# Kernel optimization log

Hardware: AMD Instinct MI355X
Metric: run time of the kernel (lower is better)

Reference implementation:

```python
import jax, jax.numpy as jnp
import numpy as np

N_NODES = 100000


def _deg_norm(idx, n):
    # inverse-sqrt degree, zero-degree nodes -> 0 (DGL norm='both' convention)
    deg = jax.ops.segment_sum(jnp.ones(idx.shape, jnp.float32), idx, num_segments=n)
    return jnp.where(deg > 0, jax.lax.rsqrt(jnp.maximum(deg, 1.0)), 0.0)


def graph_conv(x, src, dst, W, b, n):
    # symmetric normalization: D_out^{-1/2} on src, D_in^{-1/2} on dst
    norm_src = _deg_norm(src, n)  # [N]
    norm_dst = _deg_norm(dst, n)  # [N]
    h = (x * norm_src[:, None]) @ W          # apply weight first (in >= out)
    msg = h[src]                              # gather [E, out]
    agg = jax.ops.segment_sum(msg, dst, num_segments=n)  # scatter-add [N, out]
    return agg * norm_dst[:, None] + b


def setup_inputs() -> dict:
    key = jax.random.key(0)
    ks = jax.random.split(key, 6)
    x = jax.random.normal(ks[0], (N_NODES, 128), dtype=jnp.float32)
    edge_index = jax.random.randint(ks[1], (2, 1600000), 0, N_NODES, dtype=jnp.int64)
    W1 = jax.random.normal(ks[2], (128, 64), dtype=jnp.float32) * (1.0 / np.sqrt(128))
    b1 = jnp.zeros((64,), jnp.float32)
    W2 = jax.random.normal(ks[3], (64, 32), dtype=jnp.float32) * (1.0 / np.sqrt(64))
    b2 = jnp.zeros((32,), jnp.float32)
    Wl = jax.random.normal(ks[4], (32, 1), dtype=jnp.float32) * (1.0 / np.sqrt(32))
    bl = jnp.zeros((1,), jnp.float32)
    return {"x": x, "edge_index": edge_index, "W1": W1, "b1": b1,
            "W2": W2, "b2": b2, "Wl": Wl, "bl": bl}


def reference(x, edge_index, W1, b1, W2, b2, Wl, bl):
    src, dst = edge_index[0], edge_index[1]
    n = x.shape[0]
    h = graph_conv(x, src, dst, W1, b1, n)
    h = jax.nn.relu(h)
    # dropout(p=0.5) is identity at inference
    h = graph_conv(h, src, dst, W2, b2, n)
    return h @ Wl + bl  # [N, 1]
```

## Files before the change

kernel.cpp:

```cpp
#include <hip/hip_runtime.h>
#include <hip/hip_fp16.h>


#define WAVE 64
#define NRANGE 8
#define NQUAD 2
#define CB 1024

typedef _Float16 f16x8 __attribute__((ext_vector_type(8)));
typedef float f32x4 __attribute__((ext_vector_type(4)));

__global__ __launch_bounds__(256) void k_hist(const int* __restrict__ srcArr,
                                              const int* __restrict__ dstArr,
                                              unsigned* __restrict__ partial_s,
                                              unsigned* __restrict__ partial_d,
                                              int E, int B, int C, int chunkE) {
    extern __shared__ unsigned hist[];
    const int q = blockIdx.x & (NQUAD - 1);
    const int c = blockIdx.x >> 1;
    const int lo = q * 4 * B;
    const int* nodes = blockIdx.y ? dstArr : srcArr;
    unsigned* partial = blockIdx.y ? partial_d : partial_s;

    for (int b = threadIdx.x; b < B; b += 256) hist[b] = 0u;
    __syncthreads();

    const int beg = c * chunkE, end = min(beg + chunkE, E);
    const int n4 = (end - beg) >> 2;
    const int4* p = (const int4*)(nodes + beg);
    for (int j = threadIdx.x; j < n4; j += 256) {
        int4 v = p[j];
#pragma unroll
        for (int k = 0; k < 4; ++k) {
            int a = (&v.x)[k] - lo;
            if ((unsigned)a < (unsigned)(4 * B)) {
                int h2 = (a >= 2 * B);
                int r2 = a - (h2 ? 2 * B : 0);
                int h1 = (r2 >= B);
                int bin = r2 - (h1 ? B : 0);
                atomicAdd(&hist[bin], 1u << (((h2 << 1) | h1) << 3));
            }
        }
    }
    for (int j = beg + (n4 << 2) + threadIdx.x; j < end; j += 256) {
        int a = nodes[j] - lo;
        if ((unsigned)a < (unsigned)(4 * B)) {
            int h2 = (a >= 2 * B);
            int r2 = a - (h2 ? 2 * B : 0);
            int h1 = (r2 >= B);
            int bin = r2 - (h1 ? B : 0);
            atomicAdd(&hist[bin], 1u << (((h2 << 1) | h1) << 3));
        }
    }
    __syncthreads();
    unsigned* outp = partial + (size_t)(q * C + c) * B;
    for (int b = threadIdx.x; b < B; b += 256) outp[b] = hist[b];
}

__global__ __launch_bounds__(256) void k_reduce_norm(const unsigned* __restrict__ partial_s,
                                                     unsigned* __restrict__ partial_d,
                                                     float* __restrict__ norm_s,
                                                     float* __restrict__ norm_d,
                                                     unsigned* __restrict__ deg_d,
                                                     int N, int B, int C) {
    int t = blockIdx.x * 256 + threadIdx.x;
    if (t >= NQUAD * B) return;
    int q = t / B, b = t - q * B;
    size_t base = (size_t)(q * C) * B + b;
    unsigned ds = 0;
    for (int c = 0; c < C; ++c) ds += partial_s[base + (size_t)c * B];
    unsigned run = 0;
    for (int c = 0; c < C; ++c) {
        size_t ix = base + (size_t)c * B;
        unsigned v = partial_d[ix];
        partial_d[ix] = run;
        run += v;
    }
#pragma unroll
    for (int j = 0; j < 4; ++j) {
        int n = q * 4 * B + j * B + b;
        if (n < N) {
            unsigned d0 = (ds >> (8 * j)) & 0xffu;
            unsigned d1 = (run >> (8 * j)) & 0xffu;
            deg_d[n] = d1;
            norm_s[n] = d0 ? rsqrtf((float)d0) : 0.0f;
            norm_d[n] = d1 ? rsqrtf((float)d1) : 0.0f;
        }
    }
}

__global__ __launch_bounds__(256) void k_prep(const float* __restrict__ W1,
                                              const float* __restrict__ W2,
                                              const float* __restrict__ b2,
                                              const float* __restrict__ Wl,
                                              const float* __restrict__ bl,
                                              _Float16* __restrict__ wt,
                                              float* __restrict__ w2l,
                                              float* __restrict__ c0) {
    int t = threadIdx.x;
    for (int i = 0; i < 32; ++i) {
        int e = i * 256 + t;
        int k = e >> 6, n = e & 63;
        wt[n * 128 + k] = (_Float16)W1[e];
    }
    if (t < 64) {
        float acc = 0.f;
#pragma unroll
        for (int j = 0; j < 32; ++j) acc += W2[t * 32 + j] * Wl[j];
        w2l[t] = acc;
    }
    if (t == 0) {
        float s = 0.f;
#pragma unroll
        for (int j = 0; j < 32; ++j) s += b2[j] * Wl[j];
        *c0 = s + bl[0];
    }
}

__global__ __launch_bounds__(256) void k_blocksum(const unsigned* __restrict__ deg,
                                                  unsigned* __restrict__ partial, int N) {
    __shared__ unsigned sw[4];
    int i = blockIdx.x * 256 + threadIdx.x;
    unsigned v = (i < N) ? deg[i] : 0u;
#pragma unroll
    for (int off = 32; off; off >>= 1) v += __shfl_xor((int)v, off);
    if ((threadIdx.x & 63) == 0) sw[threadIdx.x >> 6] = v;
    __syncthreads();
    if (threadIdx.x == 0) partial[blockIdx.x] = sw[0] + sw[1] + sw[2] + sw[3];
}

__global__ __launch_bounds__(512) void k_scanpartial(const unsigned* __restrict__ partial,
                                                     unsigned* __restrict__ blockoff,
                                                     unsigned* __restrict__ offsets,
                                                     int nb, int N) {
    __shared__ unsigned s[512];
    int t = threadIdx.x;
    unsigned v = (t < nb) ? partial[t] : 0u;
    s[t] = v;
    __syncthreads();
    for (int off = 1; off < 512; off <<= 1) {
        unsigned a = (t >= off) ? s[t - off] : 0u;
        __syncthreads();
        s[t] += a;
        __syncthreads();
    }
    if (t < nb) blockoff[t] = s[t] - v;
    if (t == nb - 1) offsets[N] = s[t];
}

__global__ __launch_bounds__(256) void k_offsets(const unsigned* __restrict__ deg,
                                                 const unsigned* __restrict__ blockoff,
                                                 unsigned* __restrict__ offsets, int N) {
    __shared__ unsigned s[256];
    int t = threadIdx.x;
    int i = blockIdx.x * 256 + t;
    unsigned v = (i < N) ? deg[i] : 0u;
    s[t] = v;
    __syncthreads();
    for (int off = 1; off < 256; off <<= 1) {
        unsigned a = (t >= off) ? s[t - off] : 0u;
        __syncthreads();
        s[t] += a;
        __syncthreads();
    }
    if (i < N) offsets[i] = blockoff[blockIdx.x] + s[t] - v;
}

__global__ __launch_bounds__(256) void k_cnt(const int* __restrict__ dst,
                                             unsigned* __restrict__ cnt,
                                             int E, int B, int chunkEb) {
    __shared__ unsigned lc[NRANGE];
    if (threadIdx.x < NRANGE) lc[threadIdx.x] = 0u;
    __syncthreads();
    const int c = blockIdx.x;
    const int beg = c * chunkEb, end = min(beg + chunkEb, E);
    unsigned pc[NRANGE] = {};
    for (int i = beg + (int)threadIdx.x; i < end; i += 256) {
        int r = dst[i] / B;
#pragma unroll
        for (int rr = 0; rr < NRANGE; ++rr) pc[rr] += (r == rr);
    }
#pragma unroll
    for (int rr = 0; rr < NRANGE; ++rr) {
        unsigned v = pc[rr];
#pragma unroll
        for (int off = 32; off; off >>= 1) v += __shfl_xor((int)v, off);
        if ((threadIdx.x & 63) == 0 && v) atomicAdd(&lc[rr], v);
    }
    __syncthreads();
    if (threadIdx.x < NRANGE) cnt[threadIdx.x * CB + c] = lc[threadIdx.x];
}

__global__ __launch_bounds__(256) void k_scancnt2(const unsigned* __restrict__ cnt,
                                                  unsigned* __restrict__ segBase) {
    __shared__ unsigned s[256];
    const int t = threadIdx.x;
    const int PER = (NRANGE * CB) / 256;
    unsigned loc[PER];
    unsigned sum = 0;
#pragma unroll
    for (int j = 0; j < PER; ++j) { loc[j] = sum; sum += cnt[t * PER + j]; }
    s[t] = sum;
    __syncthreads();
    for (int off = 1; off < 256; off <<= 1) {
        unsigned a = (t >= off) ? s[t - off] : 0u;
        __syncthreads();
        s[t] += a;
        __syncthreads();
    }
    unsigned base = s[t] - sum;
#pragma unroll
    for (int j = 0; j < PER; ++j) segBase[t * PER + j] = base + loc[j];
    if (t == 255) segBase[NRANGE * CB] = s[255];
}

__global__ __launch_bounds__(256) void k_bucket(const int* __restrict__ src,
                                                const int* __restrict__ dst,
                                                const unsigned* __restrict__ segBase,
                                                uint2* __restrict__ ebuf,
                                                int E, int B, int chunkEb) {
    __shared__ unsigned lcnt[NRANGE];
    const int c = blockIdx.x;
    const int lane = threadIdx.x & 63;
    if (threadIdx.x < NRANGE) lcnt[threadIdx.x] = 0u;
    __syncthreads();

    unsigned sb[NRANGE];
#pragma unroll
    for (int r = 0; r < NRANGE; ++r) sb[r] = segBase[r * CB + c];

    const int beg = c * chunkEb, end = min(beg + chunkEb, E);
    for (int i = beg + (int)threadIdx.x; i < end; i += 256) {
        int d = dst[i];
        int s = src[i];
        int r = d / B;
#pragma unroll
        for (int rr = 0; rr < NRANGE; ++rr) {
            unsigned long long m = __ballot(r == rr);
            if (m) {
                int leader = __ffsll((long long)m) - 1;
                unsigned base = 0;
                if (lane == leader) base = atomicAdd(&lcnt[rr], (unsigned)__popcll(m));
                base = (unsigned)__shfl((int)base, leader);
                if (r == rr) {
                    unsigned before = (unsigned)__popcll(m & ((1ull << lane) - 1ull));
                    ebuf[sb[rr] + base + before] = make_uint2((unsigned)s, (unsigned)d);
                }
            }
        }
    }
}

__global__ __launch_bounds__(256) void k_fill2(const uint2* __restrict__ ebuf,
                                               const unsigned* __restrict__ segBase,
                                               const unsigned* __restrict__ offsets,
                                               const unsigned* __restrict__ rel,
                                               unsigned* __restrict__ csr,
                                               int N, int B, int C, int RB) {
    extern __shared__ unsigned curs[];
    const int r = blockIdx.x & (NRANGE - 1);
    const int ch = blockIdx.x >> 3;
    const int lo = r * B;
    const int bins = min(B, N - lo);
    const int sh = (r & 3) << 3;
    const unsigned* relp = rel + (size_t)((r >> 2) * C + ch) * B;
    for (int b = threadIdx.x; b < bins; b += 256)
        curs[b] = offsets[lo + b] + ((relp[b] >> sh) & 0xffu);
    __syncthreads();

    const unsigned s0 = segBase[r * CB + ch * RB];
    const unsigned s1 = segBase[r * CB + ch * RB + RB];
    for (unsigned i = s0 + threadIdx.x; i < s1; i += 256) {
        uint2 e = ebuf[i];
        int a = (int)e.y - lo;
        if ((unsigned)a < (unsigned)bins)
            csr[atomicAdd(&curs[a], 1u)] = e.x;
    }
}

__global__ __launch_bounds__(256) void k_gemm1(const float* __restrict__ x,
                                               const _Float16* __restrict__ wt,
                                               const float* __restrict__ norm_s,
                                               __half* __restrict__ h1h, int N) {
    __shared__ __align__(16) _Float16 xs[64 * 128];
    const int tid = threadIdx.x, lane = tid & 63, wv = tid >> 6;
    const int r0 = blockIdx.x * 64;

    f16x8 bf[4][4];
#pragma unroll
    for (int kt = 0; kt < 4; ++kt)
#pragma unroll
        for (int nt = 0; nt < 4; ++nt)
            bf[kt][nt] = *(const f16x8*)&wt[(nt * 16 + (lane & 15)) * 128 +
                                            kt * 32 + (lane >> 4) * 8];

#pragma unroll
    for (int it = 0; it < 8; ++it) {
        int e = it * 256 + tid;
        int r = e >> 5, c = e & 31;
        int row = r0 + r;
        float4 v = (row < N) ? ((const float4*)x)[(size_t)row * 32 + c]
                             : make_float4(0.f, 0.f, 0.f, 0.f);
        __half2 lo2 = __floats2half2_rn(v.x, v.y);
        __half2 hi2 = __floats2half2_rn(v.z, v.w);
        uint2 pk;
        pk.x = *(unsigned*)&lo2;
        pk.y = *(unsigned*)&hi2;
        int byte = r * 256 + c * 8;
        byte ^= (r & 7) << 4;
        *(uint2*)((char*)xs + byte) = pk;
    }
    __syncthreads();

    f32x4 acc[4] = {};
    const int rloc = wv * 16 + (lane & 15);
#pragma unroll
    for (int kt = 0; kt < 4; ++kt) {
        int byte = rloc * 256 + (kt * 32 + (lane >> 4) * 8) * 2;
        byte ^= (rloc & 7) << 4;
        f16x8 af = *(const f16x8*)((char*)xs + byte);
#pragma unroll
        for (int nt = 0; nt < 4; ++nt)
            acc[nt] = __builtin_amdgcn_mfma_f32_16x16x32_f16(af, bf[kt][nt], acc[nt], 0, 0, 0);
    }

#pragma unroll
    for (int j = 0; j < 4; ++j) {
        int row = r0 + wv * 16 + (lane >> 4) * 4 + j;
        if (row < N) {
            float ns = norm_s[row];
#pragma unroll
            for (int nt = 0; nt < 4; ++nt)
                h1h[(size_t)row * 64 + nt * 16 + (lane & 15)] =
                    __float2half(acc[nt][j] * ns);
        }
    }
}

__global__ __launch_bounds__(256) void k_agg_rdot(const unsigned* __restrict__ offsets,
                                                  const unsigned* __restrict__ csr,
                                                  const __half* __restrict__ h1h,
                                                  const float* __restrict__ norm_s,
                                                  const float* __restrict__ norm_d,
                                                  const float* __restrict__ b1,
                                                  const float* __restrict__ w2l,
                                                  float* __restrict__ s_node, int N) {
    const int lane = threadIdx.x & 63;
    const int slot = lane >> 4;
    const int p = lane & 15;
    const int v = (blockIdx.x * 256 + threadIdx.x) >> 6;
    if (v >= N) return;
    const unsigned beg = offsets[v], end = offsets[v + 1];

    float a0 = 0.f, a1 = 0.f, a2 = 0.f, a3 = 0.f;
#define GATHER(sreg) { \
        uint2 u = *(const uint2*)&h1h[(size_t)(sreg) * 64 + 4 * p]; \
        float2 f0 = __half22float2(*(__half2*)&u.x); \
        float2 f1 = __half22float2(*(__half2*)&u.y); \
        a0 += f0.x; a1 += f0.y; a2 += f1.x; a3 += f1.y; }

    for (unsigned base = beg; base < end; base += WAVE) {
        const int n = (int)min((unsigned)WAVE, end - base);
        int sv = (lane < n) ? (int)csr[base + lane] : 0;
        int i = 0;
        for (; i + 32 <= n; i += 32) {
            int s0 = __shfl(sv, i + 0 + slot);
            int s1 = __shfl(sv, i + 4 + slot);
            int s2 = __shfl(sv, i + 8 + slot);
            int s3 = __shfl(sv, i + 12 + slot);
            int s4 = __shfl(sv, i + 16 + slot);
            int s5 = __shfl(sv, i + 20 + slot);
            int s6 = __shfl(sv, i + 24 + slot);
            int s7 = __shfl(sv, i + 28 + slot);
            GATHER(s0); GATHER(s1); GATHER(s2); GATHER(s3);
            GATHER(s4); GATHER(s5); GATHER(s6); GATHER(s7);
        }
        for (; i + 16 <= n; i += 16) {
            int s0 = __shfl(sv, i + 0 + slot);
            int s1 = __shfl(sv, i + 4 + slot);
            int s2 = __shfl(sv, i + 8 + slot);
            int s3 = __shfl(sv, i + 12 + slot);
            GATHER(s0); GATHER(s1); GATHER(s2); GATHER(s3);
        }
        for (; i < n; i += 4) {
            int e = i + slot;
            int s = __shfl(sv, min(e, n - 1));
            if (e < n) GATHER(s);
        }
    }
#undef GATHER
    a0 += __shfl_xor(a0, 16); a0 += __shfl_xor(a0, 32);
    a1 += __shfl_xor(a1, 16); a1 += __shfl_xor(a1, 32);
    a2 += __shfl_xor(a2, 16); a2 += __shfl_xor(a2, 32);
    a3 += __shfl_xor(a3, 16); a3 += __shfl_xor(a3, 32);

    float nd = norm_d[v];
    float4 bq = *(const float4*)&b1[4 * p];
    float4 wq = *(const float4*)&w2l[4 * p];
    float t = fmaxf(fmaf(a0, nd, bq.x), 0.f) * wq.x
            + fmaxf(fmaf(a1, nd, bq.y), 0.f) * wq.y
            + fmaxf(fmaf(a2, nd, bq.z), 0.f) * wq.z
            + fmaxf(fmaf(a3, nd, bq.w), 0.f) * wq.w;
#pragma unroll
    for (int off = 8; off; off >>= 1) t += __shfl_xor(t, off);
    if (lane == 0) s_node[v] = t * norm_s[v];
}

__global__ __launch_bounds__(256) void k_out(const unsigned* __restrict__ offsets,
                                             const unsigned* __restrict__ csr,
                                             const float* __restrict__ s_node,
                                             const float* __restrict__ norm_d,
                                             const float* __restrict__ c0,
                                             float* __restrict__ out, int N) {
    int v = blockIdx.x * 256 + threadIdx.x;
    if (v >= N) return;
    unsigned beg = offsets[v], end = offsets[v + 1];
    float sum = 0.f;
    unsigned j = beg;
    for (; j + 4 <= end; j += 4) {
        float a = s_node[csr[j + 0]], b = s_node[csr[j + 1]];
        float c = s_node[csr[j + 2]], d = s_node[csr[j + 3]];
        sum += a + b + c + d;
    }
    for (; j < end; ++j) sum += s_node[csr[j]];
    out[v] = fmaf(sum, norm_d[v], *c0);
}

extern "C" void kernel_launch(void* const* d_in, const int* in_sizes, int n_in,
                              void* d_out, int out_size, void* d_ws, size_t ws_size,
                              hipStream_t stream) {
    const float* x  = (const float*)d_in[0];
    const int*   ei = (const int*)d_in[1];
    const float* W1 = (const float*)d_in[2];
    const float* b1 = (const float*)d_in[3];
    const float* W2 = (const float*)d_in[4];
    const float* b2 = (const float*)d_in[5];
    const float* Wl = (const float*)d_in[6];
    const float* bl = (const float*)d_in[7];

    const int N = in_sizes[0] / 128;
    const int E = in_sizes[1] / 2;
    const int* src = ei;
    const int* dst = ei + E;
    const int NB = (N + 255) / 256;
    const int B = (N + NRANGE - 1) / NRANGE;

    size_t baseBytes = 0;
    {
        auto pad = [](size_t b) { return (b + 255) & ~(size_t)255; };
        baseBytes = pad((size_t)N * 4) * 3 + pad((size_t)(N + 1) * 4) +
                    pad((size_t)NB * 4) * 2 + pad((size_t)N * 64 * 2) +
                    pad((size_t)E * 4) + pad((size_t)N * 4) + pad(64 * 4) + pad(4) +
                    pad(64 * 128 * 2) + pad((size_t)E * 8) +
                    pad((size_t)(NRANGE * CB + 1) * 4) * 2;
    }
    int C = 64;
    while (C > 4 && baseBytes + 2ull * NQUAD * C * B * 4ull > ws_size) C >>= 1;
    const int chunkEb = (E + CB - 1) / CB;
    const int RB = CB / C;
    const int chunkE = chunkEb * RB;

    char* w = (char*)d_ws;
    auto alloc = [&](size_t bytes) -> void* {
        void* r = (void*)w;
        w += (bytes + 255) & ~(size_t)255;
        return r;
    };
    float*    norm_s    = (float*)alloc((size_t)N * 4);
    float*    norm_d    = (float*)alloc((size_t)N * 4);
    unsigned* deg_d     = (unsigned*)alloc((size_t)N * 4);
    unsigned* offsets   = (unsigned*)alloc((size_t)(N + 1) * 4);
    unsigned* partial   = (unsigned*)alloc((size_t)NB * 4);
    unsigned* blockoff  = (unsigned*)alloc((size_t)NB * 4);
    __half*   h1h       = (__half*)alloc((size_t)N * 64 * 2);
    unsigned* csr       = (unsigned*)alloc((size_t)E * 4);
    float*    s_node    = (float*)alloc((size_t)N * 4);
    float*    w2l       = (float*)alloc(64 * 4);
    float*    c0        = (float*)alloc(4);
    _Float16* wt        = (_Float16*)alloc(64 * 128 * 2);
    uint2*    ebuf      = (uint2*)alloc((size_t)E * 8);
    unsigned* cnt       = (unsigned*)alloc((size_t)(NRANGE * CB + 1) * 4);
    unsigned* segBase   = (unsigned*)alloc((size_t)(NRANGE * CB + 1) * 4);
    unsigned* partial_s = (unsigned*)alloc((size_t)NQUAD * C * B * 4);
    unsigned* partial_d = (unsigned*)alloc((size_t)NQUAD * C * B * 4);

    float* out = (float*)d_out;
    const size_t ldsB = (size_t)B * 4;

    k_cnt<<<CB, 256, 0, stream>>>(dst, cnt, E, B, chunkEb);
    k_scancnt2<<<1, 256, 0, stream>>>(cnt, segBase);
    k_bucket<<<CB, 256, 0, stream>>>(src, dst, segBase, ebuf, E, B, chunkEb);

    k_hist<<<dim3(NQUAD * C, 2), 256, ldsB, stream>>>(src, dst, partial_s, partial_d,
                                                      E, B, C, chunkE);
    k_prep<<<1, 256, 0, stream>>>(W1, W2, b2, Wl, bl, wt, w2l, c0);

    k_reduce_norm<<<(NQUAD * B + 255) / 256, 256, 0, stream>>>(partial_s, partial_d,
                                                               norm_s, norm_d,
                                                               deg_d, N, B, C);
    k_blocksum<<<NB, 256, 0, stream>>>(deg_d, partial, N);
    k_scanpartial<<<1, 512, 0, stream>>>(partial, blockoff, offsets, NB, N);
    k_offsets<<<NB, 256, 0, stream>>>(deg_d, blockoff, offsets, N);

    k_fill2<<<NRANGE * C, 256, ldsB, stream>>>(ebuf, segBase, offsets, partial_d,
                                               csr, N, B, C, RB);

    k_gemm1<<<(N + 63) / 64, 256, 0, stream>>>(x, wt, norm_s, h1h, N);

    k_agg_rdot<<<(N + 3) / 4, 256, 0, stream>>>(offsets, csr, h1h, norm_s, norm_d,
                                                b1, w2l, s_node, N);
    k_out<<<NB, 256, 0, stream>>>(offsets, csr, s_node, norm_d, c0, out, N);
}
```

Baseline: 195.7 us.

## Fuse CSR build, degree norms, scans and GEMM1 into one cooperative kernel

Roughly ten small launches (count, bucket, histogram, reduce/norm, block scans, offsets, fill, weight prep, first GEMM) become one persistent cooperative kernel of 512 blocks, separated by grid-wide syncs. The histogram partitioning is also retuned to 16 node ranges and 32 chunks with fixed sizes, and independent phases (bucketing, block sums, GEMM tiles) share the stages between syncs. This removes launch gaps and tail idle time between dependent stages. In exchange, parallelism per phase is capped at the grid size and each grid.sync adds latency. Occupancy is also limited by the larger dynamic LDS allocation.

```diff
diff --git a/kernel.cpp b/kernel.cpp
--- a/kernel.cpp
+++ b/kernel.cpp
@@ -1,338 +1,314 @@
 #include <hip/hip_runtime.h>
 #include <hip/hip_fp16.h>
+#include <hip/hip_cooperative_groups.h>
+
+namespace cg = cooperative_groups;
 
 
 #define WAVE 64
 #define NRANGE 8
-#define NQUAD 2
 #define CB 1024
+#define GRID 512
+#define CHK 32
+#define RB (CB / CHK)
 
 typedef _Float16 f16x8 __attribute__((ext_vector_type(8)));
 typedef float f32x4 __attribute__((ext_vector_type(4)));
 
-__global__ __launch_bounds__(256) void k_hist(const int* __restrict__ srcArr,
-                                              const int* __restrict__ dstArr,
-                                              unsigned* __restrict__ partial_s,
-                                              unsigned* __restrict__ partial_d,
-                                              int E, int B, int C, int chunkE) {
-    extern __shared__ unsigned hist[];
-    const int q = blockIdx.x & (NQUAD - 1);
-    const int c = blockIdx.x >> 1;
-    const int lo = q * 4 * B;
-    const int* nodes = blockIdx.y ? dstArr : srcArr;
-    unsigned* partial = blockIdx.y ? partial_d : partial_s;
-
-    for (int b = threadIdx.x; b < B; b += 256) hist[b] = 0u;
-    __syncthreads();
-
-    const int beg = c * chunkE, end = min(beg + chunkE, E);
-    const int n4 = (end - beg) >> 2;
-    const int4* p = (const int4*)(nodes + beg);
-    for (int j = threadIdx.x; j < n4; j += 256) {
-        int4 v = p[j];
-#pragma unroll
-        for (int k = 0; k < 4; ++k) {
-            int a = (&v.x)[k] - lo;
-            if ((unsigned)a < (unsigned)(4 * B)) {
-                int h2 = (a >= 2 * B);
-                int r2 = a - (h2 ? 2 * B : 0);
-                int h1 = (r2 >= B);
-                int bin = r2 - (h1 ? B : 0);
-                atomicAdd(&hist[bin], 1u << (((h2 << 1) | h1) << 3));
-            }
-        }
-    }
-    for (int j = beg + (n4 << 2) + threadIdx.x; j < end; j += 256) {
-        int a = nodes[j] - lo;
-        if ((unsigned)a < (unsigned)(4 * B)) {
-            int h2 = (a >= 2 * B);
-            int r2 = a - (h2 ? 2 * B : 0);
-            int h1 = (r2 >= B);
-            int bin = r2 - (h1 ? B : 0);
-            atomicAdd(&hist[bin], 1u << (((h2 << 1) | h1) << 3));
-        }
-    }
-    __syncthreads();
-    unsigned* outp = partial + (size_t)(q * C + c) * B;
-    for (int b = threadIdx.x; b < B; b += 256) outp[b] = hist[b];
-}
-
-__global__ __launch_bounds__(256) void k_reduce_norm(const unsigned* __restrict__ partial_s,
-                                                     unsigned* __restrict__ partial_d,
-                                                     float* __restrict__ norm_s,
-                                                     float* __restrict__ norm_d,
-                                                     unsigned* __restrict__ deg_d,
-                                                     int N, int B, int C) {
-    int t = blockIdx.x * 256 + threadIdx.x;
-    if (t >= NQUAD * B) return;
-    int q = t / B, b = t - q * B;
-    size_t base = (size_t)(q * C) * B + b;
-    unsigned ds = 0;
-    for (int c = 0; c < C; ++c) ds += partial_s[base + (size_t)c * B];
-    unsigned run = 0;
-    for (int c = 0; c < C; ++c) {
-        size_t ix = base + (size_t)c * B;
-        unsigned v = partial_d[ix];
-        partial_d[ix] = run;
-        run += v;
-    }
-#pragma unroll
-    for (int j = 0; j < 4; ++j) {
-        int n = q * 4 * B + j * B + b;
-        if (n < N) {
-            unsigned d0 = (ds >> (8 * j)) & 0xffu;
-            unsigned d1 = (run >> (8 * j)) & 0xffu;
-            deg_d[n] = d1;
-            norm_s[n] = d0 ? rsqrtf((float)d0) : 0.0f;
-            norm_d[n] = d1 ? rsqrtf((float)d1) : 0.0f;
-        }
-    }
-}
-
-__global__ __launch_bounds__(256) void k_prep(const float* __restrict__ W1,
-                                              const float* __restrict__ W2,
-                                              const float* __restrict__ b2,
-                                              const float* __restrict__ Wl,
-                                              const float* __restrict__ bl,
-                                              _Float16* __restrict__ wt,
-                                              float* __restrict__ w2l,
-                                              float* __restrict__ c0) {
-    int t = threadIdx.x;
-    for (int i = 0; i < 32; ++i) {
-        int e = i * 256 + t;
-        int k = e >> 6, n = e & 63;
-        wt[n * 128 + k] = (_Float16)W1[e];
-    }
-    if (t < 64) {
-        float acc = 0.f;
-#pragma unroll
-        for (int j = 0; j < 32; ++j) acc += W2[t * 32 + j] * Wl[j];
-        w2l[t] = acc;
-    }
-    if (t == 0) {
-        float s = 0.f;
-#pragma unroll
-        for (int j = 0; j < 32; ++j) s += b2[j] * Wl[j];
-        *c0 = s + bl[0];
-    }
-}
-
-__global__ __launch_bounds__(256) void k_blocksum(const unsigned* __restrict__ deg,
-                                                  unsigned* __restrict__ partial, int N) {
-    __shared__ unsigned sw[4];
-    int i = blockIdx.x * 256 + threadIdx.x;
-    unsigned v = (i < N) ? deg[i] : 0u;
-#pragma unroll
-    for (int off = 32; off; off >>= 1) v += __shfl_xor((int)v, off);
-    if ((threadIdx.x & 63) == 0) sw[threadIdx.x >> 6] = v;
-    __syncthreads();
-    if (threadIdx.x == 0) partial[blockIdx.x] = sw[0] + sw[1] + sw[2] + sw[3];
-}
-
-__global__ __launch_bounds__(512) void k_scanpartial(const unsigned* __restrict__ partial,
-                                                     unsigned* __restrict__ blockoff,
-                                                     unsigned* __restrict__ offsets,
-                                                     int nb, int N) {
-    __shared__ unsigned s[512];
-    int t = threadIdx.x;
-    unsigned v = (t < nb) ? partial[t] : 0u;
-    s[t] = v;
-    __syncthreads();
-    for (int off = 1; off < 512; off <<= 1) {
-        unsigned a = (t >= off) ? s[t - off] : 0u;
-        __syncthreads();
-        s[t] += a;
-        __syncthreads();
-    }
-    if (t < nb) blockoff[t] = s[t] - v;
-    if (t == nb - 1) offsets[N] = s[t];
-}
-
-__global__ __launch_bounds__(256) void k_offsets(const unsigned* __restrict__ deg,
-                                                 const unsigned* __restrict__ blockoff,
-                                                 unsigned* __restrict__ offsets, int N) {
-    __shared__ unsigned s[256];
-    int t = threadIdx.x;
-    int i = blockIdx.x * 256 + t;
-    unsigned v = (i < N) ? deg[i] : 0u;
-    s[t] = v;
-    __syncthreads();
-    for (int off = 1; off < 256; off <<= 1) {
-        unsigned a = (t >= off) ? s[t - off] : 0u;
-        __syncthreads();
-        s[t] += a;
-        __syncthreads();
-    }
-    if (i < N) offsets[i] = blockoff[blockIdx.x] + s[t] - v;
-}
-
-__global__ __launch_bounds__(256) void k_cnt(const int* __restrict__ dst,
-                                             unsigned* __restrict__ cnt,
-                                             int E, int B, int chunkEb) {
-    __shared__ unsigned lc[NRANGE];
-    if (threadIdx.x < NRANGE) lc[threadIdx.x] = 0u;
-    __syncthreads();
-    const int c = blockIdx.x;
-    const int beg = c * chunkEb, end = min(beg + chunkEb, E);
-    unsigned pc[NRANGE] = {};
-    for (int i = beg + (int)threadIdx.x; i < end; i += 256) {
-        int r = dst[i] / B;
-#pragma unroll
-        for (int rr = 0; rr < NRANGE; ++rr) pc[rr] += (r == rr);
-    }
-#pragma unroll
-    for (int rr = 0; rr < NRANGE; ++rr) {
-        unsigned v = pc[rr];
+__global__ __launch_bounds__(256, 2) void k_build(
+    const int* __restrict__ src, const int* __restrict__ dst,
+    const float* __restrict__ x,
+    const float* __restrict__ W1, const float* __restrict__ W2,
+    const float* __restrict__ b2, const float* __restrict__ Wl,
+    const float* __restrict__ bl,
+    unsigned* cnt, unsigned* segBase, uint2* ebuf,
+    unsigned* partial_s, unsigned* partial_d,
+    float* norm_s, float* norm_d, unsigned* deg_d,
+    unsigned* partial, unsigned* blockoff, unsigned* offsets,
+    unsigned* csr, _Float16* wt, float* w2l, float* c0, __half* h1h,
+    int E, int N, int rngB, int hb, int chunkEb, int chunkE,
+    int NB, int ntiles)
+{
+    extern __shared__ unsigned lds[];
+    cg::grid_group grid = cg::this_grid();
+    const int bid = blockIdx.x;
+    const int tid = threadIdx.x;
+    const int lane = tid & 63;
+
+    for (int c = bid; c < CB; c += GRID) {
+        if (tid < NRANGE) lds[tid] = 0u;
+        __syncthreads();
+        const int beg = c * chunkEb, end = min(beg + chunkEb, E);
+        unsigned pc[NRANGE] = {};
+        for (int i = beg + tid; i < end; i += 256) {
+            int r = dst[i] / rngB;
+#pragma unroll
+            for (int rr = 0; rr < NRANGE; ++rr) pc[rr] += (r == rr);
+        }
+#pragma unroll
+        for (int rr = 0; rr < NRANGE; ++rr) {
+            unsigned v = pc[rr];
+#pragma unroll
+            for (int off = 32; off; off >>= 1) v += __shfl_xor((int)v, off);
+            if (lane == 0 && v) atomicAdd(&lds[rr], v);
+        }
+        __syncthreads();
+        if (tid < NRANGE) cnt[tid * CB + c] = lds[tid];
+        __syncthreads();
+    }
+    if (bid == GRID - 1) {
+        for (int i = 0; i < 32; ++i) {
+            int e = i * 256 + tid;
+            int k = e >> 6, n = e & 63;
+            wt[n * 128 + k] = (_Float16)W1[e];
+        }
+        if (tid < 64) {
+            float acc = 0.f;
+#pragma unroll
+            for (int j = 0; j < 32; ++j) acc += W2[tid * 32 + j] * Wl[j];
+            w2l[tid] = acc;
+        }
+        if (tid == 0) {
+            float s = 0.f;
+#pragma unroll
+            for (int j = 0; j < 32; ++j) s += b2[j] * Wl[j];
+            *c0 = s + bl[0];
+        }
+    }
+    if (bid < 256) {
+        const int arr = bid >> 7;
+        const int hq  = (bid >> 5) & 3;
+        const int c   = bid & 31;
+        const int lo  = hq * 4 * hb;
+        const int span = 4 * hb;
+        const int* nodes = arr ? dst : src;
+        unsigned* po = (arr ? partial_d : partial_s) + (size_t)(hq * CHK + c) * hb;
+        for (int b = tid; b < hb; b += 256) lds[b] = 0u;
+        __syncthreads();
+        const int beg = c * chunkE, end = min(beg + chunkE, E);
+        const int n4 = (end - beg) >> 2;
+        const int4* p = (const int4*)(nodes + beg);
+        for (int j = tid; j < n4; j += 256) {
+            int4 v = p[j];
+#pragma unroll
+            for (int k = 0; k < 4; ++k) {
+                int a = (&v.x)[k] - lo;
+                if ((unsigned)a < (unsigned)span) {
+                    int jj = a / hb;
+                    int b = a - jj * hb;
+                    atomicAdd(&lds[b], 1u << (jj << 3));
+                }
+            }
+        }
+        for (int j2 = beg + (n4 << 2) + tid; j2 < end; j2 += 256) {
+            int a = nodes[j2] - lo;
+            if ((unsigned)a < (unsigned)span) {
+                int jj = a / hb;
+                int b = a - jj * hb;
+                atomicAdd(&lds[b], 1u << (jj << 3));
+            }
+        }
+        __syncthreads();
+        for (int b = tid; b < hb; b += 256) po[b] = lds[b];
+    }
+    grid.sync();
+
+    if (bid == 0) {
+        const int PER = (NRANGE * CB) / 256;
+        unsigned loc[PER];
+        unsigned sum = 0;
+#pragma unroll
+        for (int j = 0; j < PER; ++j) { loc[j] = sum; sum += cnt[tid * PER + j]; }
+        lds[tid] = sum;
+        __syncthreads();
+        for (int off = 1; off < 256; off <<= 1) {
+            unsigned a = (tid >= off) ? lds[tid - off] : 0u;
+            __syncthreads();
+            lds[tid] += a;
+            __syncthreads();
+        }
+        unsigned base = lds[tid] - sum;
+#pragma unroll
+        for (int j = 0; j < PER; ++j) segBase[tid * PER + j] = base + loc[j];
+        if (tid == 255) segBase[NRANGE * CB] = lds[255];
+    } else {
+        int t = (bid - 1) * 256 + tid;
+        if (t < 4 * hb) {
+            int hq = t / hb, b = t - hq * hb;
+            size_t base = (size_t)(hq * CHK) * hb + b;
+            unsigned ds = 0;
+            for (int c = 0; c < CHK; ++c) ds += partial_s[base + (size_t)c * hb];
+            unsigned run = 0;
+            for (int c = 0; c < CHK; ++c) {
+                size_t ix = base + (size_t)c * hb;
+                unsigned v = partial_d[ix];
+                partial_d[ix] = run;
+                run += v;
+            }
+#pragma unroll
+            for (int j = 0; j < 4; ++j) {
+                int n = hq * 4 * hb + j * hb + b;
+                if (n < N) {
+                    unsigned d0 = (ds >> (8 * j)) & 0xffu;
+                    unsigned d1 = (run >> (8 * j)) & 0xffu;
+                    deg_d[n] = d1;
+                    norm_s[n] = d0 ? rsqrtf((float)d0) : 0.0f;
+                    norm_d[n] = d1 ? rsqrtf((float)d1) : 0.0f;
+                }
+            }
+        }
+    }
+    grid.sync();
+
+    for (int c = bid; c < CB; c += GRID) {
+        if (tid < NRANGE) lds[tid] = 0u;
+        __syncthreads();
+        unsigned sb[NRANGE];
+#pragma unroll
+        for (int r = 0; r < NRANGE; ++r) sb[r] = segBase[r * CB + c];
+        const int beg = c * chunkEb, end = min(beg + chunkEb, E);
+        for (int i = beg + tid; i < end; i += 256) {
+            int d = dst[i], s = src[i];
+            int r = d / rngB;
+#pragma unroll
+            for (int rr = 0; rr < NRANGE; ++rr) {
+                unsigned long long m = __ballot(r == rr);
+                if (m) {
+                    int leader = __ffsll((long long)m) - 1;
+                    unsigned b2r = 0;
+                    if (lane == leader) b2r = atomicAdd(&lds[rr], (unsigned)__popcll(m));
+                    b2r = (unsigned)__shfl((int)b2r, leader);
+                    if (r == rr) {
+                        unsigned before = (unsigned)__popcll(m & ((1ull << lane) - 1ull));
+                        ebuf[sb[rr] + b2r + before] = make_uint2((unsigned)s, (unsigned)d);
+                    }
+                }
+            }
+        }
+        __syncthreads();
+    }
+    for (int t = bid; t < NB; t += GRID) {
+        int i = t * 256 + tid;
+        unsigned v = (i < N) ? deg_d[i] : 0u;
 #pragma unroll
         for (int off = 32; off; off >>= 1) v += __shfl_xor((int)v, off);
-        if ((threadIdx.x & 63) == 0 && v) atomicAdd(&lc[rr], v);
-    }
-    __syncthreads();
-    if (threadIdx.x < NRANGE) cnt[threadIdx.x * CB + c] = lc[threadIdx.x];
-}
-
-__global__ __launch_bounds__(256) void k_scancnt2(const unsigned* __restrict__ cnt,
-                                                  unsigned* __restrict__ segBase) {
-    __shared__ unsigned s[256];
-    const int t = threadIdx.x;
-    const int PER = (NRANGE * CB) / 256;
-    unsigned loc[PER];
-    unsigned sum = 0;
-#pragma unroll
-    for (int j = 0; j < PER; ++j) { loc[j] = sum; sum += cnt[t * PER + j]; }
-    s[t] = sum;
-    __syncthreads();
-    for (int off = 1; off < 256; off <<= 1) {
-        unsigned a = (t >= off) ? s[t - off] : 0u;
-        __syncthreads();
-        s[t] += a;
-        __syncthreads();
-    }
-    unsigned base = s[t] - sum;
-#pragma unroll
-    for (int j = 0; j < PER; ++j) segBase[t * PER + j] = base + loc[j];
-    if (t == 255) segBase[NRANGE * CB] = s[255];
-}
-
-__global__ __launch_bounds__(256) void k_bucket(const int* __restrict__ src,
-                                                const int* __restrict__ dst,
-                                                const unsigned* __restrict__ segBase,
-                                                uint2* __restrict__ ebuf,
-                                                int E, int B, int chunkEb) {
-    __shared__ unsigned lcnt[NRANGE];
-    const int c = blockIdx.x;
-    const int lane = threadIdx.x & 63;
-    if (threadIdx.x < NRANGE) lcnt[threadIdx.x] = 0u;
-    __syncthreads();
-
-    unsigned sb[NRANGE];
-#pragma unroll
-    for (int r = 0; r < NRANGE; ++r) sb[r] = segBase[r * CB + c];
-
-    const int beg = c * chunkEb, end = min(beg + chunkEb, E);
-    for (int i = beg + (int)threadIdx.x; i < end; i += 256) {
-        int d = dst[i];
-        int s = src[i];
-        int r = d / B;
-#pragma unroll
-        for (int rr = 0; rr < NRANGE; ++rr) {
-            unsigned long long m = __ballot(r == rr);
-            if (m) {
-                int leader = __ffsll((long long)m) - 1;
-                unsigned base = 0;
-                if (lane == leader) base = atomicAdd(&lcnt[rr], (unsigned)__popcll(m));
-                base = (unsigned)__shfl((int)base, leader);
-                if (r == rr) {
-                    unsigned before = (unsigned)__popcll(m & ((1ull << lane) - 1ull));
-                    ebuf[sb[rr] + base + before] = make_uint2((unsigned)s, (unsigned)d);
+        __syncthreads();
+        if ((tid & 63) == 0) lds[tid >> 6] = v;
+        __syncthreads();
+        if (tid == 0) partial[t] = lds[0] + lds[1] + lds[2] + lds[3];
+        __syncthreads();
+    }
+    {
+        _Float16* xs = (_Float16*)lds;
+        for (int tile = bid; tile < ntiles; tile += GRID) {
+            const int wv = tid >> 6;
+            const int r0 = tile * 64;
+            f16x8 bf[4][4];
+#pragma unroll
+            for (int kt = 0; kt < 4; ++kt)
+#pragma unroll
+                for (int nt = 0; nt < 4; ++nt)
+                    bf[kt][nt] = *(const f16x8*)&wt[(nt * 16 + (lane & 15)) * 128 +
+                                                    kt * 32 + (lane >> 4) * 8];
+            __syncthreads();
+#pragma unroll
+            for (int it = 0; it < 8; ++it) {
+                int e = it * 256 + tid;
+                int r = e >> 5, cc = e & 31;
+                int row = r0 + r;
+                float4 v = (row < N) ? ((const float4*)x)[(size_t)row * 32 + cc]
+                                     : make_float4(0.f, 0.f, 0.f, 0.f);
+                __half2 lo2 = __floats2half2_rn(v.x, v.y);
+                __half2 hi2 = __floats2half2_rn(v.z, v.w);
+                uint2 pk;
+                pk.x = *(unsigned*)&lo2;
+                pk.y = *(unsigned*)&hi2;
+                int byte = r * 256 + cc * 8;
+                byte ^= (r & 7) << 4;
+                *(uint2*)((char*)xs + byte) = pk;
+            }
+            __syncthreads();
+            f32x4 acc[4] = {};
+            const int rloc = wv * 16 + (lane & 15);
+#pragma unroll
+            for (int kt = 0; kt < 4; ++kt) {
+                int byte = rloc * 256 + (kt * 32 + (lane >> 4) * 8) * 2;
+                byte ^= (rloc & 7) << 4;
+                f16x8 af = *(const f16x8*)((char*)xs + byte);
+#pragma unroll
+                for (int nt = 0; nt < 4; ++nt)
+                    acc[nt] = __builtin_amdgcn_mfma_f32_16x16x32_f16(af, bf[kt][nt], acc[nt], 0, 0, 0);
+            }
+#pragma unroll
+            for (int j = 0; j < 4; ++j) {
+                int row = r0 + wv * 16 + (lane >> 4) * 4 + j;
+                if (row < N) {
+                    float ns = norm_s[row];
+#pragma unroll
+                    for (int nt = 0; nt < 4; ++nt)
+                        h1h[(size_t)row * 64 + nt * 16 + (lane & 15)] =
+                            __float2half(acc[nt][j] * ns);
                 }
             }
-        }
-    }
-}
-
-__global__ __launch_bounds__(256) void k_fill2(const uint2* __restrict__ ebuf,
-                                               const unsigned* __restrict__ segBase,
-                                               const unsigned* __restrict__ offsets,
-                                               const unsigned* __restrict__ rel,
-                                               unsigned* __restrict__ csr,
-                                               int N, int B, int C, int RB) {
-    extern __shared__ unsigned curs[];
-    const int r = blockIdx.x & (NRANGE - 1);
-    const int ch = blockIdx.x >> 3;
-    const int lo = r * B;
-    const int bins = min(B, N - lo);
-    const int sh = (r & 3) << 3;
-    const unsigned* relp = rel + (size_t)((r >> 2) * C + ch) * B;
-    for (int b = threadIdx.x; b < bins; b += 256)
-        curs[b] = offsets[lo + b] + ((relp[b] >> sh) & 0xffu);
-    __syncthreads();
-
-    const unsigned s0 = segBase[r * CB + ch * RB];
-    const unsigned s1 = segBase[r * CB + ch * RB + RB];
-    for (unsigned i = s0 + threadIdx.x; i < s1; i += 256) {
-        uint2 e = ebuf[i];
-        int a = (int)e.y - lo;
-        if ((unsigned)a < (unsigned)bins)
-            csr[atomicAdd(&curs[a], 1u)] = e.x;
-    }
-}
-
-__global__ __launch_bounds__(256) void k_gemm1(const float* __restrict__ x,
-                                               const _Float16* __restrict__ wt,
-                                               const float* __restrict__ norm_s,
-                                               __half* __restrict__ h1h, int N) {
-    __shared__ __align__(16) _Float16 xs[64 * 128];
-    const int tid = threadIdx.x, lane = tid & 63, wv = tid >> 6;
-    const int r0 = blockIdx.x * 64;
-
-    f16x8 bf[4][4];
-#pragma unroll
-    for (int kt = 0; kt < 4; ++kt)
-#pragma unroll
-        for (int nt = 0; nt < 4; ++nt)
-            bf[kt][nt] = *(const f16x8*)&wt[(nt * 16 + (lane & 15)) * 128 +
-                                            kt * 32 + (lane >> 4) * 8];
-
-#pragma unroll
-    for (int it = 0; it < 8; ++it) {
-        int e = it * 256 + tid;
-        int r = e >> 5, c = e & 31;
-        int row = r0 + r;
-        float4 v = (row < N) ? ((const float4*)x)[(size_t)row * 32 + c]
-                             : make_float4(0.f, 0.f, 0.f, 0.f);
-        __half2 lo2 = __floats2half2_rn(v.x, v.y);
-        __half2 hi2 = __floats2half2_rn(v.z, v.w);
-        uint2 pk;
-        pk.x = *(unsigned*)&lo2;
-        pk.y = *(unsigned*)&hi2;
-        int byte = r * 256 + c * 8;
-        byte ^= (r & 7) << 4;
-        *(uint2*)((char*)xs + byte) = pk;
-    }
-    __syncthreads();
-
-    f32x4 acc[4] = {};
-    const int rloc = wv * 16 + (lane & 15);
-#pragma unroll
-    for (int kt = 0; kt < 4; ++kt) {
-        int byte = rloc * 256 + (kt * 32 + (lane >> 4) * 8) * 2;
-        byte ^= (rloc & 7) << 4;
-        f16x8 af = *(const f16x8*)((char*)xs + byte);
-#pragma unroll
-        for (int nt = 0; nt < 4; ++nt)
-            acc[nt] = __builtin_amdgcn_mfma_f32_16x16x32_f16(af, bf[kt][nt], acc[nt], 0, 0, 0);
-    }
-
-#pragma unroll
-    for (int j = 0; j < 4; ++j) {
-        int row = r0 + wv * 16 + (lane >> 4) * 4 + j;
-        if (row < N) {
-            float ns = norm_s[row];
-#pragma unroll
-            for (int nt = 0; nt < 4; ++nt)
-                h1h[(size_t)row * 64 + nt * 16 + (lane & 15)] =
-                    __float2half(acc[nt][j] * ns);
+            __syncthreads();
+        }
+    }
+    grid.sync();
+
+    if (bid == 0) {
+        unsigned p0 = (2 * tid < NB) ? partial[2 * tid] : 0u;
+        unsigned p1 = (2 * tid + 1 < NB) ? partial[2 * tid + 1] : 0u;
+        unsigned sum = p0 + p1;
+        lds[tid] = sum;
+        __syncthreads();
+        for (int off = 1; off < 256; off <<= 1) {
+            unsigned a = (tid >= off) ? lds[tid - off] : 0u;
+            __syncthreads();
+            lds[tid] += a;
+            __syncthreads();
+        }
+        unsigned excl = lds[tid] - sum;
+        if (2 * tid < NB) blockoff[2 * tid] = excl;
+        if (2 * tid + 1 < NB) blockoff[2 * tid + 1] = excl + p0;
+        if (tid == 255) offsets[N] = lds[255];
+    }
+    grid.sync();
+
+    for (int t = bid; t < NB; t += GRID) {
+        int i = t * 256 + tid;
+        unsigned v = (i < N) ? deg_d[i] : 0u;
+        __syncthreads();
+        lds[tid] = v;
+        __syncthreads();
+        for (int off = 1; off < 256; off <<= 1) {
+            unsigned a = (tid >= off) ? lds[tid - off] : 0u;
+            __syncthreads();
+            lds[tid] += a;
+            __syncthreads();
+        }
+        if (i < N) offsets[i] = blockoff[t] + lds[tid] - v;
+        __syncthreads();
+    }
+    grid.sync();
+
+    {
+        const int hr = bid & 15;
+        const int ch = bid >> 4;
+        const int r  = hr >> 1;
+        const int lo = hr * hb;
+        const int bins = min(hb, N - lo);
+        const int hq = hr >> 2, sh = (hr & 3) << 3;
+        const unsigned* relp = partial_d + (size_t)(hq * CHK + ch) * hb;
+        for (int b = tid; b < bins; b += 256)
+            lds[b] = offsets[lo + b] + ((relp[b] >> sh) & 0xffu);
+        __syncthreads();
+        const unsigned s0 = segBase[r * CB + ch * RB];
+        const unsigned s1 = segBase[r * CB + ch * RB + RB];
+        for (unsigned i = s0 + tid; i < s1; i += 256) {
+            uint2 e = ebuf[i];
+            int a = (int)e.y - lo;
+            if ((unsigned)a < (unsigned)bins)
+                csr[atomicAdd(&lds[a], 1u)] = e.x;
         }
     }
 }
@@ -420,7 +396,7 @@
     for (; j + 4 <= end; j += 4) {
         float a = s_node[csr[j + 0]], b = s_node[csr[j + 1]];
         float c = s_node[csr[j + 2]], d = s_node[csr[j + 3]];
-        sum += a + b + c + d;
+        sum += (a + b) + (c + d);
     }
     for (; j < end; ++j) sum += s_node[csr[j]];
     out[v] = fmaf(sum, norm_d[v], *c0);
@@ -438,27 +414,16 @@
     const float* Wl = (const float*)d_in[6];
     const float* bl = (const float*)d_in[7];
 
-    const int N = in_sizes[0] / 128;
-    const int E = in_sizes[1] / 2;
+    int N = in_sizes[0] / 128;
+    int E = in_sizes[1] / 2;
     const int* src = ei;
     const int* dst = ei + E;
-    const int NB = (N + 255) / 256;
-    const int B = (N + NRANGE - 1) / NRANGE;
-
-    size_t baseBytes = 0;
-    {
-        auto pad = [](size_t b) { return (b + 255) & ~(size_t)255; };
-        baseBytes = pad((size_t)N * 4) * 3 + pad((size_t)(N + 1) * 4) +
-                    pad((size_t)NB * 4) * 2 + pad((size_t)N * 64 * 2) +
-                    pad((size_t)E * 4) + pad((size_t)N * 4) + pad(64 * 4) + pad(4) +
-                    pad(64 * 128 * 2) + pad((size_t)E * 8) +
-                    pad((size_t)(NRANGE * CB + 1) * 4) * 2;
-    }
-    int C = 64;
-    while (C > 4 && baseBytes + 2ull * NQUAD * C * B * 4ull > ws_size) C >>= 1;
-    const int chunkEb = (E + CB - 1) / CB;
-    const int RB = CB / C;
-    const int chunkE = chunkEb * RB;
+    int NB = (N + 255) / 256;
+    int hb = (N + 15) / 16;
+    int rngB = 2 * hb;
+    int chunkEb = (E + CB - 1) / CB;
+    int chunkE = chunkEb * RB;
+    int ntiles = (N + 63) / 64;
 
     char* w = (char*)d_ws;
     auto alloc = [&](size_t bytes) -> void* {
@@ -481,33 +446,29 @@
     uint2*    ebuf      = (uint2*)alloc((size_t)E * 8);
     unsigned* cnt       = (unsigned*)alloc((size_t)(NRANGE * CB + 1) * 4);
     unsigned* segBase   = (unsigned*)alloc((size_t)(NRANGE * CB + 1) * 4);
-    unsigned* partial_s = (unsigned*)alloc((size_t)NQUAD * C * B * 4);
-    unsigned* partial_d = (unsigned*)alloc((size_t)NQUAD * C * B * 4);
+    unsigned* partial_s = (unsigned*)alloc((size_t)4 * CHK * hb * 4);
+    unsigned* partial_d = (unsigned*)alloc((size_t)4 * CHK * hb * 4);
 
     float* out = (float*)d_out;
-    const size_t ldsB = (size_t)B * 4;
-
-    k_cnt<<<CB, 256, 0, stream>>>(dst, cnt, E, B, chunkEb);
-    k_scancnt2<<<1, 256, 0, stream>>>(cnt, segBase);
-    k_bucket<<<CB, 256, 0, stream>>>(src, dst, segBase, ebuf, E, B, chunkEb);
-
-    k_hist<<<dim3(NQUAD * C, 2), 256, ldsB, stream>>>(src, dst, partial_s, partial_d,
-                                                      E, B, C, chunkE);
-    k_prep<<<1, 256, 0, stream>>>(W1, W2, b2, Wl, bl, wt, w2l, c0);
-
-    k_reduce_norm<<<(NQUAD * B + 255) / 256, 256, 0, stream>>>(partial_s, partial_d,
-                                                               norm_s, norm_d,
-                                                               deg_d, N, B, C);
-    k_blocksum<<<NB, 256, 0, stream>>>(deg_d, partial, N);
-    k_scanpartial<<<1, 512, 0, stream>>>(partial, blockoff, offsets, NB, N);
-    k_offsets<<<NB, 256, 0, stream>>>(deg_d, blockoff, offsets, N);
-
-    k_fill2<<<NRANGE * C, 256, ldsB, stream>>>(ebuf, segBase, offsets, partial_d,
-                                               csr, N, B, C, RB);
-
-    k_gemm1<<<(N + 63) / 64, 256, 0, stream>>>(x, wt, norm_s, h1h, N);
-
-    k_agg_rdot<<<(N + 3) / 4, 256, 0, stream>>>(offsets, csr, h1h, norm_s, norm_d,
-                                                b1, w2l, s_node, N);
+    size_t ldsB = (size_t)hb * 4;
+    if (ldsB < 16384) ldsB = 16384;
+    ldsB = (ldsB + 255) & ~(size_t)255;
+
+    void* args[] = {
+        (void*)&src, (void*)&dst, (void*)&x, (void*)&W1, (void*)&W2,
+        (void*)&b2, (void*)&Wl, (void*)&bl,
+        (void*)&cnt, (void*)&segBase, (void*)&ebuf,
+        (void*)&partial_s, (void*)&partial_d,
+        (void*)&norm_s, (void*)&norm_d, (void*)&deg_d,
+        (void*)&partial, (void*)&blockoff, (void*)&offsets,
+        (void*)&csr, (void*)&wt, (void*)&w2l, (void*)&c0, (void*)&h1h,
+        (void*)&E, (void*)&N, (void*)&rngB, (void*)&hb,
+        (void*)&chunkEb, (void*)&chunkE, (void*)&NB, (void*)&ntiles
+    };
+    hipLaunchCooperativeKernel((const void*)k_build, dim3(GRID), dim3(256),
+                               args, (unsigned)ldsB, stream);
+
+    k_agg_rdot<<<(N + 3) / 4, 256, 0, stream>>>(offsets, csr, h1h, norm_s,
+                                                norm_d, b1, w2l, s_node, N);
     k_out<<<NB, 256, 0, stream>>>(offsets, csr, s_node, norm_d, c0, out, N);
 }
```

Result: slower. 461.4 us (+135.8%).
